# Kernel tuning notes

Hardware: AMD Instinct MI355X
Metric: run time of the kernel (lower is better)

## Reference

```python
import jax, jax.numpy as jnp
import numpy as np
from itertools import combinations

N_QUBITS = 8
N_TRASH = 2
N_LAYERS = 4
BATCH = 32768
DIM = 2 ** N_QUBITS  # 256


def _cz_pairs():
    # same CZ pattern as layer() in the torch module; all pairs are distinct,
    # and CZ gates are diagonal and commute, so they fuse into one sign mask.
    pairs = list(combinations(range(N_TRASH), 2))
    for idx in range(N_TRASH):
        for i in range(N_TRASH):
            for j in range(N_TRASH + i, N_QUBITS, N_TRASH):
                pairs.append(((idx + i) % N_TRASH, j))
    return pairs


def _cz_layer_sign():
    bits = np.indices((2,) * N_QUBITS)  # [n_qubits, 2,...,2]; wire 0 = MSB (PennyLane order)
    sign = np.ones((2,) * N_QUBITS, np.float32)
    for a, b in _cz_pairs():
        sign = sign * (1.0 - 2.0 * (bits[a] * bits[b]).astype(np.float32))
    return jnp.asarray(sign)[None]  # broadcast over batch

_CZ_SIGN = _cz_layer_sign()


def _ry(state, theta, w):
    # RY(theta) on wire w, batched over leading axis. state: [B,2,...,2] complex64
    c = jnp.cos(theta / 2).astype(jnp.complex64)
    s = jnp.sin(theta / 2).astype(jnp.complex64)
    g = jnp.stack([jnp.stack([c, -s]), jnp.stack([s, c])])  # [2,2]
    out = jnp.tensordot(g, state, axes=((1,), (1 + w,)))
    return jnp.moveaxis(out, 0, 1 + w)


def _axis_vec(vals, w):
    shape = [1] * (N_QUBITS + 1)
    shape[1 + w] = 2
    return jnp.asarray(vals, dtype=jnp.complex64).reshape(shape)


def _apply_pauli(state, w, p):
    if p == 'X':
        return jnp.flip(state, axis=1 + w)
    if p == 'Y':
        return jnp.flip(state, axis=1 + w) * _axis_vec([-1j, 1j], w)
    return state * _axis_vec([1.0 + 0j, -1.0 + 0j], w)  # Z


def _forward(x, weights):
    # AmplitudeEmbedding(normalize=True)
    norm = jnp.sqrt(jnp.sum(x * x, axis=-1, keepdims=True))
    psi = (x / norm).astype(jnp.complex64).reshape((-1,) + (2,) * N_QUBITS)
    for l in range(N_LAYERS - 1):
        for q in range(N_QUBITS):
            psi = _ry(psi, weights[l * N_QUBITS + q], q)
        psi = psi * _CZ_SIGN  # all CZs of the layer fused into one diagonal
    base = (N_LAYERS - 1) * N_QUBITS
    for q in range(N_TRASH):  # last_layer: RY on trash qubits only
        psi = _ry(psi, weights[base + q], q)

    axes = tuple(range(1, N_QUBITS + 1))
    conj_psi = jnp.conj(psi)

    def ev(op_state):
        return jnp.sum(conj_psi * op_state, axis=axes).real.astype(jnp.float32)

    w0, w1 = 6, 7
    terms = [
        ev(_apply_pauli(psi, w0, 'X')),
        ev(_apply_pauli(psi, w0, 'Y')),
        ev(_apply_pauli(psi, w0, 'Z')),
        ev(_apply_pauli(psi, w1, 'X')),
        ev(_apply_pauli(psi, w1, 'Y')),
        ev(_apply_pauli(psi, w1, 'Z')),
        ev(_apply_pauli(_apply_pauli(psi, w0, 'X'), w1, 'X')),
        ev(_apply_pauli(_apply_pauli(psi, w0, 'Y'), w1, 'Y')),
        ev(_apply_pauli(_apply_pauli(psi, w0, 'Z'), w1, 'Z')),
    ]
    return jnp.stack(terms, axis=1)  # [B, 9]


def setup_inputs() -> dict:
    key = jax.random.key(0)
    kx, kw = jax.random.split(key)
    x = jax.random.normal(kx, (BATCH, DIM), dtype=jnp.float32)
    n_w = N_LAYERS * N_QUBITS - (N_QUBITS - N_TRASH)  # 26
    weights = jax.random.normal(kw, (n_w,), dtype=jnp.float32)
    return {'x': x, 'weights': weights}


def reference(x, weights):
    return _forward(x, weights)
```

## Files before the change

### kernel.cpp

```cpp
#include <hip/hip_runtime.h>
#include <math.h>

#define DIM 256

__global__ void trig_kernel(const float* __restrict__ w, float* __restrict__ ws) {
    int t = threadIdx.x;
    if (t < 26) {
        float h = 0.5f * w[t];
        ws[t]      = cosf(h);
        ws[26 + t] = sinf(h);
    }
}

template<int B>
__device__ __forceinline__ void ry_bit(float* v, float c, float s) {
#pragma unroll
    for (int i = 0; i < 32; ++i) {
        if (!(i & (1 << B))) {
            const int j = i | (1 << B);
            float lo = v[i], hi = v[j];
            v[i] = fmaf(-s, hi, c * lo);
            v[j] = fmaf(s, lo, c * hi);
        }
    }
}

__device__ __forceinline__ void cz_A(float* v, float fE, float fO) {
#pragma unroll
    for (int i = 0; i < 32; ++i) v[i] *= (__popc(i) & 1) ? fO : fE;
}

__device__ __forceinline__ void cz_B(float* v, float pB, float nB) {
#pragma unroll
    for (int j = 0; j < 32; ++j) {
        const int w0 = (j >> 4) & 1, w1 = (j >> 3) & 1;
        const int ip = __popc(j & 7) & 1;
        if (w0 & w1)      v[j] = -v[j];
        else if (w0 ^ w1) v[j] *= ip ? nB : pB;
    }
}

__device__ __forceinline__ void tA2B(float* v, float4* W, int l3) {
#pragma unroll
    for (int k = 0; k < 8; ++k)
        W[l3 * 8 + (k ^ l3)] = make_float4(v[4*k], v[4*k+1], v[4*k+2], v[4*k+3]);
#pragma unroll
    for (int g = 0; g < 8; ++g) {
        float4 f = W[g * 8 + (l3 ^ g)];
        v[4*g] = f.x; v[4*g+1] = f.y; v[4*g+2] = f.z; v[4*g+3] = f.w;
    }
}

__device__ __forceinline__ void tB2A(float* v, float4* W, int l3) {
#pragma unroll
    for (int g = 0; g < 8; ++g)
        W[g * 8 + (l3 ^ g)] = make_float4(v[4*g], v[4*g+1], v[4*g+2], v[4*g+3]);
#pragma unroll
    for (int k = 0; k < 8; ++k) {
        float4 f = W[l3 * 8 + (k ^ l3)];
        v[4*k] = f.x; v[4*k+1] = f.y; v[4*k+2] = f.z; v[4*k+3] = f.w;
    }
}

__global__ __launch_bounds__(256) void qae_kernel(const float* __restrict__ x,
                                                  const float* __restrict__ tw,
                                                  float* __restrict__ out,
                                                  int batch) {
    __shared__ float4 lds4[2048];
    const int lane = threadIdx.x & 63;
    const int wave = blockIdx.x * 4 + (threadIdx.x >> 6);
    const int l3   = lane & 7;
    const int e    = lane >> 3;
    const int eb   = wave * 8 + e;
    float4* W = lds4 + (threadIdx.x >> 6) * 512 + e * 64;

    const float* CW = tw;
    const float* SW = tw + 26;

    const int a_w0 = (l3 >> 2) & 1, a_w1 = (l3 >> 1) & 1, a_w2 = l3 & 1;
    const int aa = a_w0 & a_w1, dd = a_w0 ^ a_w1;
    const float fE = (aa ^ (dd & a_w2)) ? -1.f : 1.f;
    const float fO = ((aa ^ (dd & a_w2)) ^ dd) ? -1.f : 1.f;
    const float pB = (__popc(l3) & 1) ? -1.f : 1.f;
    const float nB = -pB;

    float v[32];
    if (eb < batch) {
        const float* xp = x + (size_t)eb * DIM + l3 * 32;
#pragma unroll
        for (int k = 0; k < 8; ++k) {
            float4 f = *(const float4*)(xp + 4 * k);
            v[4*k] = f.x; v[4*k+1] = f.y; v[4*k+2] = f.z; v[4*k+3] = f.w;
        }
    } else {
#pragma unroll
        for (int i = 0; i < 32; ++i) v[i] = 0.f;
    }
    float nrm2 = 0.f;
#pragma unroll
    for (int i = 0; i < 32; ++i) nrm2 = fmaf(v[i], v[i], nrm2);

#define RY(b, g) ry_bit<b>(v, CW[g], SW[g])
    RY(4, 3); RY(3, 4); RY(2, 5); RY(1, 6); RY(0, 7);
    tA2B(v, W, l3);
    RY(4, 0); RY(3, 1); RY(2, 2);
    cz_B(v, pB, nB);
    RY(4, 8); RY(3, 9); RY(2, 10);
    tB2A(v, W, l3);
    RY(4, 11); RY(3, 12); RY(2, 13); RY(1, 14); RY(0, 15);
    cz_A(v, fE, fO);
    RY(4, 19); RY(3, 20); RY(2, 21); RY(1, 22); RY(0, 23);
    tA2B(v, W, l3);
    RY(4, 16); RY(3, 17); RY(2, 18);
    cz_B(v, pB, nB);
    RY(4, 24); RY(3, 25);
#undef RY

    float X6 = 0, X7 = 0, XX = 0, YY = 0, Z6 = 0, Z7 = 0, ZZ = 0;
#pragma unroll
    for (int g = 0; g < 8; ++g) {
        float q0 = v[4*g], q1 = v[4*g+1], q2 = v[4*g+2], q3 = v[4*g+3];
        X6 += q0*q2 + q1*q3;
        X7 += q0*q1 + q2*q3;
        XX += q0*q3 + q1*q2;
        YY += q1*q2 - q0*q3;
        float s0 = q0*q0, s1 = q1*q1, s2 = q2*q2, s3 = q3*q3;
        Z6 += s0 + s1 - s2 - s3;
        Z7 += s0 - s1 + s2 - s3;
        ZZ += s0 - s1 - s2 + s3;
    }
    X6 *= 2.f; X7 *= 2.f; XX *= 2.f; YY *= 2.f;

#pragma unroll
    for (int m = 1; m < 8; m <<= 1) {
        nrm2 += __shfl_xor(nrm2, m);
        X6 += __shfl_xor(X6, m);  X7 += __shfl_xor(X7, m);
        XX += __shfl_xor(XX, m);  YY += __shfl_xor(YY, m);
        Z6 += __shfl_xor(Z6, m);  Z7 += __shfl_xor(Z7, m);
        ZZ += __shfl_xor(ZZ, m);
    }

    if (eb < batch) {
        const float inv = 1.f / nrm2;
        float* o = out + (size_t)eb * 9;
        const int t = l3;
        if (t < 7) {
            float val = (t == 0) ? X6 : (t == 1) ? Z6 : (t == 2) ? X7
                      : (t == 3) ? Z7 : (t == 4) ? XX : (t == 5) ? YY : ZZ;
            int off = t + (t >= 1 ? 1 : 0) + (t >= 3 ? 1 : 0);
            o[off] = val * inv;
        } else {
            o[1] = 0.f;
            o[4] = 0.f;
        }
    }
}

extern "C" void kernel_launch(void* const* d_in, const int* in_sizes, int n_in,
                              void* d_out, int out_size, void* d_ws, size_t ws_size,
                              hipStream_t stream) {
    const float* x = (const float*)d_in[0];
    const float* w = (const float*)d_in[1];
    float* out = (float*)d_out;
    float* ws  = (float*)d_ws;
    const int batch = in_sizes[0] / DIM;

    trig_kernel<<<1, 64, 0, stream>>>(w, ws);

    const int waves  = (batch + 7) / 8;
    const int blocks = (waves + 3) / 4;
    qae_kernel<<<blocks, 256, 0, stream>>>(x, ws, out, batch);
}
```

Measured before the change: 84.49 us.

## Fuse trig into main kernel, pack state as float2, drop gates that cannot affect outputs

Removes the separate trig kernel: each wave computes cos/sin of the needed half-angles with fast intrinsics and broadcasts them through readlane. The per-thread state is held as packed float2 pairs so rotations can use packed FP32 math, and the load layout is changed so one LDS transpose is removed. Rotations on wires that cannot affect the measured observables (several trash-layer gates) are dropped and the gate order is rearranged using commutation. This cuts the extra launch, one LDS round trip and part of the ALU work. The cost is reliance on __cosf/__sinf precision and on the correctness of the reordering.

```diff
diff --git a/kernel.cpp b/kernel.cpp
--- a/kernel.cpp
+++ b/kernel.cpp
@@ -2,68 +2,37 @@
 #include <math.h>
 
 #define DIM 256
+typedef float v2f __attribute__((ext_vector_type(2)));
 
-__global__ void trig_kernel(const float* __restrict__ w, float* __restrict__ ws) {
-    int t = threadIdx.x;
-    if (t < 26) {
-        float h = 0.5f * w[t];
-        ws[t]      = cosf(h);
-        ws[26 + t] = sinf(h);
-    }
+__device__ __forceinline__ v2f mk2(float a, float b) { v2f r; r.x = a; r.y = b; return r; }
+
+__device__ __forceinline__ float rl(float v, int l) {
+    return __uint_as_float(__builtin_amdgcn_readlane(__float_as_uint(v), l));
 }
 
-template<int B>
-__device__ __forceinline__ void ry_bit(float* v, float c, float s) {
+template<int B2>
+__device__ __forceinline__ void ry_pk(v2f* v, float c, float s) {
 #pragma unroll
-    for (int i = 0; i < 32; ++i) {
-        if (!(i & (1 << B))) {
-            const int j = i | (1 << B);
-            float lo = v[i], hi = v[j];
-            v[i] = fmaf(-s, hi, c * lo);
-            v[j] = fmaf(s, lo, c * hi);
+    for (int p = 0; p < 16; ++p)
+        if (!(p & (1 << B2))) {
+            const int q = p | (1 << B2);
+            v2f lo = v[p], hi = v[q];
+            v[p] = c * lo - s * hi;
+            v[q] = s * lo + c * hi;
         }
-    }
 }
 
-__device__ __forceinline__ void cz_A(float* v, float fE, float fO) {
+__device__ __forceinline__ void ry_intra(v2f* v, float c, float s) {
 #pragma unroll
-    for (int i = 0; i < 32; ++i) v[i] *= (__popc(i) & 1) ? fO : fE;
-}
-
-__device__ __forceinline__ void cz_B(float* v, float pB, float nB) {
-#pragma unroll
-    for (int j = 0; j < 32; ++j) {
-        const int w0 = (j >> 4) & 1, w1 = (j >> 3) & 1;
-        const int ip = __popc(j & 7) & 1;
-        if (w0 & w1)      v[j] = -v[j];
-        else if (w0 ^ w1) v[j] *= ip ? nB : pB;
-    }
-}
-
-__device__ __forceinline__ void tA2B(float* v, float4* W, int l3) {
-#pragma unroll
-    for (int k = 0; k < 8; ++k)
-        W[l3 * 8 + (k ^ l3)] = make_float4(v[4*k], v[4*k+1], v[4*k+2], v[4*k+3]);
-#pragma unroll
-    for (int g = 0; g < 8; ++g) {
-        float4 f = W[g * 8 + (l3 ^ g)];
-        v[4*g] = f.x; v[4*g+1] = f.y; v[4*g+2] = f.z; v[4*g+3] = f.w;
-    }
-}
-
-__device__ __forceinline__ void tB2A(float* v, float4* W, int l3) {
-#pragma unroll
-    for (int g = 0; g < 8; ++g)
-        W[g * 8 + (l3 ^ g)] = make_float4(v[4*g], v[4*g+1], v[4*g+2], v[4*g+3]);
-#pragma unroll
-    for (int k = 0; k < 8; ++k) {
-        float4 f = W[l3 * 8 + (k ^ l3)];
-        v[4*k] = f.x; v[4*k+1] = f.y; v[4*k+2] = f.z; v[4*k+3] = f.w;
+    for (int p = 0; p < 16; ++p) {
+        float lo = v[p].x, hi = v[p].y;
+        v[p].x = fmaf(-s, hi, c * lo);
+        v[p].y = fmaf(s, lo, c * hi);
     }
 }
 
 __global__ __launch_bounds__(256) void qae_kernel(const float* __restrict__ x,
-                                                  const float* __restrict__ tw,
+                                                  const float* __restrict__ w,
                                                   float* __restrict__ out,
                                                   int batch) {
     __shared__ float4 lds4[2048];
@@ -74,56 +43,87 @@
     const int eb   = wave * 8 + e;
     float4* W = lds4 + (threadIdx.x >> 6) * 512 + e * 64;
 
-    const float* CW = tw;
-    const float* SW = tw + 26;
+    float h = 0.f;
+    if (lane < 20) h = 0.5f * w[lane < 18 ? lane : lane + 4];
+    const float cv = __cosf(h), sv = __sinf(h);
+#define RYP(B2, slot) ry_pk<B2>(v, rl(cv, slot), rl(sv, slot))
+#define RYI(slot)     ry_intra(v, rl(cv, slot), rl(sv, slot))
 
-    const int a_w0 = (l3 >> 2) & 1, a_w1 = (l3 >> 1) & 1, a_w2 = l3 & 1;
-    const int aa = a_w0 & a_w1, dd = a_w0 ^ a_w1;
-    const float fE = (aa ^ (dd & a_w2)) ? -1.f : 1.f;
-    const float fO = ((aa ^ (dd & a_w2)) ^ dd) ? -1.f : 1.f;
+    const int a0 = (l3 >> 2) & 1, a1 = (l3 >> 1) & 1, a2 = l3 & 1;
+    const int aa = a0 & a1, dd = a0 ^ a1;
+    const float fE = (aa ^ (dd & a2)) ? -1.f : 1.f;
+    const float fO = ((aa ^ (dd & a2)) ^ dd) ? -1.f : 1.f;
     const float pB = (__popc(l3) & 1) ? -1.f : 1.f;
-    const float nB = -pB;
+    const v2f mA0 = mk2(fE, fO), mA1 = mk2(fO, fE);
+    const v2f mBp = mk2(pB, -pB);
 
-    float v[32];
+    v2f v[16];
     if (eb < batch) {
-        const float* xp = x + (size_t)eb * DIM + l3 * 32;
+        const float* xp = x + (size_t)eb * DIM + l3 * 4;
 #pragma unroll
-        for (int k = 0; k < 8; ++k) {
-            float4 f = *(const float4*)(xp + 4 * k);
-            v[4*k] = f.x; v[4*k+1] = f.y; v[4*k+2] = f.z; v[4*k+3] = f.w;
+        for (int u = 0; u < 8; ++u) {
+            float4 f = *(const float4*)(xp + u * 32);
+            v[2 * u]     = mk2(f.x, f.y);
+            v[2 * u + 1] = mk2(f.z, f.w);
         }
     } else {
 #pragma unroll
-        for (int i = 0; i < 32; ++i) v[i] = 0.f;
+        for (int p = 0; p < 16; ++p) v[p] = mk2(0.f, 0.f);
     }
     float nrm2 = 0.f;
 #pragma unroll
-    for (int i = 0; i < 32; ++i) nrm2 = fmaf(v[i], v[i], nrm2);
+    for (int p = 0; p < 16; ++p) nrm2 += v[p].x * v[p].x + v[p].y * v[p].y;
 
-#define RY(b, g) ry_bit<b>(v, CW[g], SW[g])
-    RY(4, 3); RY(3, 4); RY(2, 5); RY(1, 6); RY(0, 7);
-    tA2B(v, W, l3);
-    RY(4, 0); RY(3, 1); RY(2, 2);
-    cz_B(v, pB, nB);
-    RY(4, 8); RY(3, 9); RY(2, 10);
-    tB2A(v, W, l3);
-    RY(4, 11); RY(3, 12); RY(2, 13); RY(1, 14); RY(0, 15);
-    cz_A(v, fE, fO);
-    RY(4, 19); RY(3, 20); RY(2, 21); RY(1, 22); RY(0, 23);
-    tA2B(v, W, l3);
-    RY(4, 16); RY(3, 17); RY(2, 18);
-    cz_B(v, pB, nB);
-    RY(4, 24); RY(3, 25);
-#undef RY
+    RYP(3, 0); RYP(2, 1); RYP(1, 2);
+
+#pragma unroll
+    for (int g = 0; g < 8; ++g)
+        W[g * 8 + (l3 ^ g)] = make_float4(v[2*g].x, v[2*g].y, v[2*g+1].x, v[2*g+1].y);
+#pragma unroll
+    for (int k = 0; k < 8; ++k) {
+        float4 f = W[l3 * 8 + (k ^ l3)];
+        v[2 * k] = mk2(f.x, f.y); v[2 * k + 1] = mk2(f.z, f.w);
+    }
+
+    RYP(3, 3); RYP(2, 4); RYP(1, 5); RYP(0, 6); RYI(7);
+#pragma unroll
+    for (int p = 0; p < 16; ++p) v[p] *= (__popc(p) & 1) ? mA1 : mA0;
+    RYP(3, 11); RYP(2, 12); RYP(1, 13); RYP(0, 14); RYI(15);
+
+#pragma unroll
+    for (int k = 0; k < 8; ++k)
+        W[l3 * 8 + (k ^ l3)] = make_float4(v[2*k].x, v[2*k].y, v[2*k+1].x, v[2*k+1].y);
+#pragma unroll
+    for (int g = 0; g < 8; ++g) {
+        float4 f = W[g * 8 + (l3 ^ g)];
+        v[2 * g] = mk2(f.x, f.y); v[2 * g + 1] = mk2(f.z, f.w);
+    }
+
+    RYP(3, 8); RYP(2, 9); RYP(1, 10);
+#pragma unroll
+    for (int p = 0; p < 16; ++p) {
+        const int w0 = (p >> 3) & 1, w1 = (p >> 2) & 1;
+        if (w0 & w1)      v[p] = -v[p];
+        else if (w0 ^ w1) v[p] *= (__popc(p & 3) & 1) ? -mBp : mBp;
+    }
+    RYP(3, 16); RYP(2, 17); RYP(0, 18); RYI(19);
+#pragma unroll
+    for (int p = 0; p < 16; ++p) {
+        const int w0 = (p >> 3) & 1, w1 = (p >> 2) & 1;
+        if (w0 & w1)      v[p] = -v[p];
+        else if (w0 ^ w1) v[p] *= (__popc(p & 3) & 1) ? -mBp : mBp;
+    }
+#undef RYP
+#undef RYI
 
     float X6 = 0, X7 = 0, XX = 0, YY = 0, Z6 = 0, Z7 = 0, ZZ = 0;
 #pragma unroll
     for (int g = 0; g < 8; ++g) {
-        float q0 = v[4*g], q1 = v[4*g+1], q2 = v[4*g+2], q3 = v[4*g+3];
-        X6 += q0*q2 + q1*q3;
-        X7 += q0*q1 + q2*q3;
-        XX += q0*q3 + q1*q2;
-        YY += q1*q2 - q0*q3;
+        float q0 = v[2*g].x, q1 = v[2*g].y, q2 = v[2*g+1].x, q3 = v[2*g+1].y;
+        X6 += q0 * q2 + q1 * q3;
+        X7 += q0 * q1 + q2 * q3;
+        XX += q0 * q3 + q1 * q2;
+        YY += q1 * q2 - q0 * q3;
         float s0 = q0*q0, s1 = q1*q1, s2 = q2*q2, s3 = q3*q3;
         Z6 += s0 + s1 - s2 - s3;
         Z7 += s0 - s1 + s2 - s3;
@@ -162,12 +162,9 @@
     const float* x = (const float*)d_in[0];
     const float* w = (const float*)d_in[1];
     float* out = (float*)d_out;
-    float* ws  = (float*)d_ws;
     const int batch = in_sizes[0] / DIM;
-
-    trig_kernel<<<1, 64, 0, stream>>>(w, ws);
 
     const int waves  = (batch + 7) / 8;
     const int blocks = (waves + 3) / 4;
-    qae_kernel<<<blocks, 256, 0, stream>>>(x, ws, out, batch);
+    qae_kernel<<<blocks, 256, 0, stream>>>(x, w, out, batch);
 }
```

After: 79.62 us. -5.8%, faster.
